# Optimization experiments

Measured on AMD Instinct MI355X. Metric: run time of the kernel, lower is better.

The kernel has to match this reference:

```python
import jax, jax.numpy as jnp
import numpy as np
from jax import lax

G = 8      # deform groups (weight groups == offset groups)
K = 3      # kernel size
K2 = K * K


def conv3x3(x, w, b):
    # NCHW, 3x3, stride 1, padding 1 (SAME)
    y = lax.conv_general_dilated(x, w, (1, 1), 'SAME',
                                 dimension_numbers=('NCHW', 'OIHW', 'NCHW'))
    return y + b[None, :, None, None]


def deform_conv2d(ref, offsets, w, b):
    # ref: [B,C,H,W], offsets: [B,2*G*K2,H,W] (torchvision layout: per group,
    # per kernel position, (dy, dx) pairs), w: [C_out, C_in/G, K, K], b: [C_out]
    B, C, H, W = ref.shape
    Cg = C // G
    off = offsets.reshape(B, G, K2, 2, H, W)
    dy = off[:, :, :, 0]  # [B,G,K2,H,W]
    dx = off[:, :, :, 1]
    ky = (jnp.arange(K2) // K - K // 2).astype(ref.dtype)  # kernel y offsets (pad=1)
    kx = (jnp.arange(K2) % K - K // 2).astype(ref.dtype)
    base_y = jnp.arange(H, dtype=ref.dtype)[:, None] + ky[:, None, None]  # [K2,H,1]
    base_x = jnp.arange(W, dtype=ref.dtype)[None, :] + kx[:, None, None]  # [K2,1,W]
    py = dy + base_y  # [B,G,K2,H,W]
    px = dx + base_x

    y0 = jnp.floor(py).astype(jnp.int32)
    x0 = jnp.floor(px).astype(jnp.int32)
    ly = py - y0.astype(ref.dtype)
    lx = px - x0.astype(ref.dtype)

    ref_flat = ref.reshape(B, G, Cg, H * W)

    def gather(yi, xi):
        valid = (yi >= 0) & (yi < H) & (xi >= 0) & (xi < W)
        idx = jnp.clip(yi, 0, H - 1) * W + jnp.clip(xi, 0, W - 1)  # [B,G,K2,H,W]
        vals = jnp.take_along_axis(ref_flat, idx.reshape(B, G, 1, K2 * H * W), axis=3)
        vals = vals.reshape(B, G, Cg, K2, H, W)
        return vals * valid[:, :, None].astype(ref.dtype)

    w00 = ((1 - ly) * (1 - lx))[:, :, None]
    w01 = ((1 - ly) * lx)[:, :, None]
    w10 = (ly * (1 - lx))[:, :, None]
    w11 = (ly * lx)[:, :, None]
    sampled = (w00 * gather(y0, x0) + w01 * gather(y0, x0 + 1)
               + w10 * gather(y0 + 1, x0) + w11 * gather(y0 + 1, x0 + 1))
    # grouped accumulation: weight [C_out, Cg, K, K] -> [G, OCg, Cg, K2]
    wg = w.reshape(G, C // G, Cg, K2)
    out = jnp.einsum('bgikhw,goik->bgohw', sampled, wg)
    return out.reshape(B, C, H, W) + b[None, :, None, None]


def setup_inputs() -> dict:
    key = jax.random.key(0)
    ks = jax.random.split(key, 10)
    B, C, H, W = 2, 64, 256, 256
    s64 = 1.0 / np.sqrt(C * 9)
    s128 = 1.0 / np.sqrt(128 * 9)
    return {
        'offset': jax.random.normal(ks[0], (B, C, H, W), jnp.float32),
        'ref': jax.random.normal(ks[1], (B, C, H, W), jnp.float32),
        'w_off': jax.random.normal(ks[2], (2 * K2 * G, C, K, K), jnp.float32) * s64,
        'b_off': jnp.zeros((2 * K2 * G,), jnp.float32),
        'w_def': jax.random.normal(ks[3], (C, C // G, K, K), jnp.float32) * (1.0 / np.sqrt((C // G) * 9)),
        'b_def': jnp.zeros((C,), jnp.float32),
        'w_r1': jax.random.normal(ks[4], (C, 2 * C, K, K), jnp.float32) * s128,
        'b_r1': jnp.zeros((C,), jnp.float32),
        'w_r2': jax.random.normal(ks[5], (C, C, K, K), jnp.float32) * s64,
        'b_r2': jnp.zeros((C,), jnp.float32),
    }


def reference(offset, ref, w_off, b_off, w_def, b_def, w_r1, b_r1, w_r2, b_r2):
    deform_offsets = conv3x3(offset, w_off, b_off)              # [B,144,H,W]
    aligned_ref = deform_conv2d(ref, deform_offsets, w_def, b_def)
    x = jnp.concatenate([ref, aligned_ref], axis=1)             # [B,128,H,W]
    x = jax.nn.relu(conv3x3(x, w_r1, b_r1))
    x = jax.nn.relu(conv3x3(x, w_r2, b_r2))
    return x + aligned_ref
```

## Files before the change

kernel.cpp:

```cpp
#include <hip/hip_runtime.h>

typedef __attribute__((ext_vector_type(8)))  short  short8;
typedef __attribute__((ext_vector_type(4)))  float  float4v;
typedef __attribute__((ext_vector_type(16))) float  float16v;
typedef __attribute__((ext_vector_type(2)))  float  f32x2;

constexpr int HH = 256, WW = 256;
constexpr int PD = 258;
constexpr int PR = 260;
constexpr size_t HWsz = (size_t)HH * WW;

__device__ inline unsigned short f2bf(float f) {
    unsigned int u = __builtin_bit_cast(unsigned int, f);
    u += 0x7FFFu + ((u >> 16) & 1u);
    return (unsigned short)(u >> 16);
}
__device__ inline float bfhalf(unsigned int w, int hi) {
    return __builtin_bit_cast(float, hi ? (w & 0xFFFF0000u) : (w << 16));
}
__device__ inline f32x2 unpk2(unsigned int w) {
    f32x2 r;
    r.x = __builtin_bit_cast(float, w << 16);
    r.y = __builtin_bit_cast(float, w & 0xFFFF0000u);
    return r;
}
__device__ inline f32x2 splat2(float s) { f32x2 r; r.x = s; r.y = s; return r; }

template<int CDST, bool WRITE_G>
__global__ __launch_bounds__(256) void nchw_to_nhwc(
    const float* __restrict__ src, unsigned short* __restrict__ dst,
    unsigned short* __restrict__ dst_g)
{
    const int px = threadIdx.x, h = blockIdx.x, bi = blockIdx.y;
    const float* s = src + (size_t)bi * 64 * HWsz + (size_t)h * WW + px;
    unsigned short* d = dst + (((size_t)bi * PD + (h + 1)) * PD + (px + 1)) * CDST;
#pragma unroll
    for (int cg = 0; cg < 8; ++cg) {
        float v[8];
#pragma unroll
        for (int j = 0; j < 8; ++j) v[j] = s[(size_t)(cg * 8 + j) * HWsz];
        uint4 pk;
        pk.x = f2bf(v[0]) | ((unsigned)f2bf(v[1]) << 16);
        pk.y = f2bf(v[2]) | ((unsigned)f2bf(v[3]) << 16);
        pk.z = f2bf(v[4]) | ((unsigned)f2bf(v[5]) << 16);
        pk.w = f2bf(v[6]) | ((unsigned)f2bf(v[7]) << 16);
        *(uint4*)&d[cg * 8] = pk;
        if (WRITE_G) {
            unsigned short* dg = dst_g +
                ((size_t)(bi * 8 + cg) * PR * PR + (size_t)(h + 1) * PR + (px + 1)) * 8;
            *(uint4*)dg = pk;
        }
    }
}

__global__ __launch_bounds__(256) void zero_border(
    unsigned short* __restrict__ p_off, unsigned short* __restrict__ p_cat,
    unsigned short* __restrict__ p_x1, unsigned short* __restrict__ refg)
{
    const int bi = blockIdx.y, which = blockIdx.z;
    if (which == 3) {
        const int total = 8 * 1548;
        for (int i = blockIdx.x * 256 + threadIdx.x; i < total; i += gridDim.x * 256) {
            int g = i / 1548, t = i - g * 1548;
            int r, c;
            if (t < 780)  { int rr = t / 260; c = t - rr * 260; r = rr == 0 ? 0 : 256 + rr; }
            else          { int u = t - 780; int cc = u >> 8; r = 1 + (u & 255); c = cc == 0 ? 0 : 256 + cc; }
            uint4 z = {0, 0, 0, 0};
            *(uint4*)&refg[((size_t)(bi * 8 + g) * PR * PR + (size_t)r * PR + c) * 8] = z;
        }
        return;
    }
    unsigned short* buf = which == 0 ? p_off : (which == 1 ? p_cat : p_x1);
    const int CIN = (which == 1) ? 128 : 64;
    const int NG = CIN / 8;
    unsigned short* p = buf + (size_t)bi * PD * PD * CIN;
    const int total = 1028 * 16;
    for (int i = blockIdx.x * 256 + threadIdx.x; i < total; i += gridDim.x * 256) {
        int g = i & 15;
        if (g >= NG) continue;
        int pxi = i >> 4;
        int r, c;
        if (pxi < 258)       { r = 0;   c = pxi; }
        else if (pxi < 516)  { r = 257; c = pxi - 258; }
        else if (pxi < 772)  { r = pxi - 516 + 1; c = 0; }
        else                 { r = pxi - 772 + 1; c = 257; }
        uint4 z = {0, 0, 0, 0};
        *(uint4*)&p[((size_t)r * PD + c) * CIN + g * 8] = z;
    }
}

__device__ inline void pack_one(const float* __restrict__ w, short* __restrict__ wpk,
                                int Cout, int Cin, int e)
{
    int j = e & 7;
    int lane = (e >> 3) & 63;
    int ksp = 9 * (Cin / 16);
    int kstep = (e >> 9) % ksp;
    int cot = (e >> 9) / ksp;
    int tap = kstep / (Cin / 16);
    int ci = (kstep % (Cin / 16)) * 16 + (lane >> 5) * 8 + j;
    int co = cot * 32 + (lane & 31);
    float v = (co < Cout) ? w[((size_t)co * Cin + ci) * 9 + tap] : 0.f;
    wpk[e] = (short)f2bf(v);
}

__global__ __launch_bounds__(256) void pack_all(
    const float* __restrict__ w1, short* __restrict__ d1,
    const float* __restrict__ w2, short* __restrict__ d2,
    const float* __restrict__ w3, short* __restrict__ d3)
{
    int e = blockIdx.x * 256 + threadIdx.x;
    if (e < 110592)               pack_one(w1, d1, 144, 64, e);
    else if (e < 110592 + 73728)  pack_one(w2, d2, 64, 128, e - 110592);
    else if (e < 221184)          pack_one(w3, d3, 64, 64,  e - 184320);
}

template<int CIN, int COF, int COTB, int MODE, int MINW>
__global__ __launch_bounds__(256, MINW) void conv_mfma_nb(
    const unsigned short* __restrict__ src,
    const short* __restrict__ wpk,
    const float* __restrict__ bias,
    unsigned short* __restrict__ dst_bf,
    float* __restrict__ dst_f,
    const unsigned short* __restrict__ resid_bf)
{
    constexpr int CHUNKS = CIN / 32;
    constexpr int KST = 9 * (CIN / 16);
    constexpr int WSEG = 3 * 4 * 66 * 8;

    __shared__ unsigned short lds[4 * WSEG];

    const int tid  = threadIdx.x;
    const int lane = tid & 63;
    const int wv   = tid >> 6;
    const int half = lane >> 5;
    const int n32  = lane & 31;
    const int h  = blockIdx.x;
    const int bi = blockIdx.y / COTB;
    const int cb = blockIdx.y % COTB;
    const int cbase = cb * COF * 32;

    unsigned short* my = lds + wv * WSEG;
    const unsigned short* srcB = src + (size_t)bi * PD * PD * CIN;
    const short8* wbase = (const short8*)wpk;

    float16v acc[COF][2];
#pragma unroll
    for (int f = 0; f < COF; ++f) {
        float16v bv;
#pragma unroll
        for (int reg = 0; reg < 16; ++reg) {
            int co = cbase + f * 32 + (reg >> 2) * 8 + 4 * half + (reg & 3);
            float b = 0.f;
            if (MODE != 0 || co < 144) b = bias[co];
            bv[reg] = b;
        }
        acc[f][0] = bv;
        acc[f][1] = bv;
    }

    for (int ch = 0; ch < CHUNKS; ++ch) {
        const unsigned short* gband = srcB + ((size_t)h * PD + wv * 64) * CIN + ch * 32;
#pragma unroll
        for (int i0 = 0; i0 < 264; i0 += 64) {
            int i = i0 + lane;
            if (i0 + 64 > 264 && i >= 264) continue;
            int px = i >> 2, o = i & 3;
#pragma unroll
            for (int r = 0; r < 3; ++r) {
                uint4 v = *(const uint4*)(gband + ((size_t)r * PD + px) * CIN + o * 8);
                *(uint4*)&my[(((size_t)r * 4 + o) * 66 + px) * 8] = v;
            }
        }

        short8 abuf[3][COF];
#pragma unroll
        for (int p = 0; p < 2; ++p) {
            const int kp = (p >> 1) * (CIN / 16) + ch * 2 + (p & 1);
#pragma unroll
            for (int f = 0; f < COF; ++f)
                abuf[p][f] = wbase[((size_t)(cb * COF + f) * KST + kp) * 64 + lane];
        }
#pragma unroll
        for (int t = 0; t < 18; ++t) {
            const int tap = t >> 1, s = t & 1;
            const int row = tap / 3, dxo = tap % 3;
            if (t + 2 < 18) {
                const int t2 = t + 2;
                const int k2 = (t2 >> 1) * (CIN / 16) + ch * 2 + (t2 & 1);
#pragma unroll
                for (int f = 0; f < COF; ++f)
                    abuf[t2 % 3][f] = wbase[((size_t)(cb * COF + f) * KST + k2) * 64 + lane];
            }
#pragma unroll
            for (int nt = 0; nt < 2; ++nt) {
                short8 b = *(const short8*)
                    &my[(((size_t)row * 4 + s * 2 + half) * 66 + nt * 32 + dxo + n32) * 8];
#pragma unroll
                for (int f = 0; f < COF; ++f)
                    acc[f][nt] = __builtin_amdgcn_mfma_f32_32x32x16_bf16(abuf[t % 3][f], b, acc[f][nt], 0, 0, 0);
            }
        }
    }

#pragma unroll
    for (int f = 0; f < COF; ++f) {
#pragma unroll
        for (int nt = 0; nt < 2; ++nt) {
            const int px = wv * 64 + nt * 32 + n32;
            float16v a = acc[f][nt];
#pragma unroll
            for (int q = 0; q < 4; ++q) {
                const int co4 = cbase + f * 32 + q * 8 + 4 * half;
                float v0 = a[q * 4 + 0], v1 = a[q * 4 + 1];
                float v2 = a[q * 4 + 2], v3 = a[q * 4 + 3];
                if (MODE == 0) {
                    if (co4 < 144) {
                        unsigned g = ((unsigned)co4 * 3641u) >> 16;
                        unsigned c = (unsigned)co4 - g * 18u;
                        unsigned lo = f2bf(v0) | ((unsigned)f2bf(v1) << 16);
                        unsigned hi = f2bf(v2) | ((unsigned)f2bf(v3) << 16);
                        unsigned short* rec = dst_bf +
                            (((size_t)(bi * 8 + g) * HWsz) + (size_t)h * WW + px) * 18;
                        if (c <= 14) {
                            *(unsigned*)&rec[c]     = lo;
                            *(unsigned*)&rec[c + 2] = hi;
                        } else {
                            *(unsigned*)&rec[16] = lo;
                            unsigned short* rec2 = dst_bf +
                                (((size_t)(bi * 8 + g + 1) * HWsz) + (size_t)h * WW + px) * 18;
                            *(unsigned*)&rec2[0] = hi;
                        }
                    }
                } else if (MODE == 1) {
                    unsigned short* d = dst_bf + (size_t)bi * PD * PD * 64;
                    uint2 pk;
                    pk.x = f2bf(fmaxf(v0, 0.f)) | ((unsigned)f2bf(fmaxf(v1, 0.f)) << 16);
                    pk.y = f2bf(fmaxf(v2, 0.f)) | ((unsigned)f2bf(fmaxf(v3, 0.f)) << 16);
                    *(uint2*)&d[(((size_t)h + 1) * PD + (px + 1)) * 64 + co4] = pk;
                } else {
                    const unsigned short* rp = resid_bf + (size_t)bi * PD * PD * 128;
                    uint2 rv = *(const uint2*)&rp[(((size_t)h + 1) * PD + (px + 1)) * 128 + 64 + co4];
                    float r0 = bfhalf(rv.x, 0), r1 = bfhalf(rv.x, 1);
                    float r2 = bfhalf(rv.y, 0), r3 = bfhalf(rv.y, 1);
                    float* d = dst_f + (size_t)bi * 64 * HWsz + (size_t)h * WW + px;
                    d[(size_t)(co4 + 0) * HWsz] = fmaxf(v0, 0.f) + r0;
                    d[(size_t)(co4 + 1) * HWsz] = fmaxf(v1, 0.f) + r1;
                    d[(size_t)(co4 + 2) * HWsz] = fmaxf(v2, 0.f) + r2;
                    d[(size_t)(co4 + 3) * HWsz] = fmaxf(v3, 0.f) + r3;
                }
            }
        }
    }
}

#define DTAP(DWK, HF, ACC)                                                    \
    {                                                                         \
        float dy = bfhalf(DWK, 0);                                            \
        float dx = bfhalf(DWK, 1);                                            \
        float py  = dy + ((HF) + (float)(k / 3 - 1));                         \
        float pxs = dx + (pxf + (float)(k % 3 - 1));                          \
        py  = fminf(fmaxf(py,  -1.f), 256.f);                                 \
        pxs = fminf(fmaxf(pxs, -1.f), 256.f);                                 \
        float fy = floorf(py), fx = floorf(pxs);                              \
        float ly = py - fy, lx = pxs - fx;                                    \
        int i00 = ((int)fy + 1) * PR + ((int)fx + 1);                         \
        float omly = 1.f - ly, omlx = 1.f - lx;                               \
        f32x2 W00 = splat2(omly * omlx), W01 = splat2(omly * lx);             \
        f32x2 W10 = splat2(ly * omlx),  W11 = splat2(ly * lx);                \
        const uint4 q00 = *(const uint4*)(rb + (size_t)i00 * 8);              \
        const uint4 q01 = *(const uint4*)(rb + (size_t)(i00 + 1) * 8);        \
        const uint4 q10 = *(const uint4*)(rb + (size_t)(i00 + PR) * 8);       \
        const uint4 q11 = *(const uint4*)(rb + (size_t)(i00 + PR + 1) * 8);   \
        union U { uint4 v; unsigned int a[4]; };                              \
        U u00{q00}, u01{q01}, u10{q10}, u11{q11};                             \
        _Pragma("unroll")                                                     \
        for (int cw = 0; cw < 4; ++cw) {                                      \
            f32x2 sv = unpk2(u00.a[cw]) * W00;                                \
            sv = __builtin_elementwise_fma(unpk2(u01.a[cw]), W01, sv);        \
            sv = __builtin_elementwise_fma(unpk2(u10.a[cw]), W10, sv);        \
            sv = __builtin_elementwise_fma(unpk2(u11.a[cw]), W11, sv);        \
            f32x2 bx = splat2(sv.x);                                          \
            f32x2 by = splat2(sv.y);                                          \
            const f32x2* wpa = (const f32x2*)&wsm2[((k * 8) + cw * 2) * 8];   \
            const f32x2* wpb = (const f32x2*)&wsm2[((k * 8) + cw * 2 + 1) * 8];\
            _Pragma("unroll")                                                 \
            for (int o = 0; o < 4; ++o) {                                     \
                ACC[o] = __builtin_elementwise_fma(wpa[o], bx, ACC[o]);       \
                ACC[o] = __builtin_elementwise_fma(wpb[o], by, ACC[o]);       \
            }                                                                 \
        }                                                                     \
    }

__global__ __launch_bounds__(256) void deform_k11(
    const unsigned short* __restrict__ refg,
    const unsigned short* __restrict__ doff,
    const float* __restrict__ wdef, const float* __restrict__ bdef,
    unsigned short* __restrict__ pcat_out)
{
    __shared__ float wsm2[576];
    const int L = blockIdx.x;
    const int xcd = L & 7;
    const int j = L >> 3;
    const int g = j & 7;
    const int r = (j >> 3) & 15;
    const int bi = j >> 7;
    const int h0 = xcd * 32 + r * 2;
    const int px = threadIdx.x;

    for (int i = threadIdx.x; i < 576; i += 256) {
        int o = i & 7, c = (i >> 3) & 7, k = i >> 6;
        wsm2[i] = wdef[(size_t)g * 576 + o * 72 + c * 9 + k];
    }
    __syncthreads();

    const unsigned int* dpA = (const unsigned int*)(
        doff + (((size_t)(bi * 8 + g) * HWsz) + (size_t)h0 * WW + px) * 18);
    const unsigned int* dpB = (const unsigned int*)(
        doff + (((size_t)(bi * 8 + g) * HWsz) + (size_t)(h0 + 1) * WW + px) * 18);
    unsigned int dwA[9], dwB[9];
#pragma unroll
    for (int k = 0; k < 9; ++k) dwA[k] = dpA[k];
#pragma unroll
    for (int k = 0; k < 9; ++k) dwB[k] = dpB[k];

    f32x2 accA[4], accB[4];
#pragma unroll
    for (int o = 0; o < 4; ++o) {
        accA[o].x = bdef[g * 8 + 2 * o];
        accA[o].y = bdef[g * 8 + 2 * o + 1];
        accB[o] = accA[o];
    }

    const unsigned short* rb = refg + (size_t)(bi * 8 + g) * PR * PR * 8;
    const float hfA = (float)h0, hfB = (float)(h0 + 1), pxf = (float)px;

#pragma unroll
    for (int k = 0; k < 9; ++k) {
        DTAP(dwA[k], hfA, accA)
        DTAP(dwB[k], hfB, accB)
    }

    unsigned short* poA = pcat_out + (((size_t)bi * PD + (h0 + 1)) * PD + (px + 1)) * 128 + 64 + g * 8;
    unsigned short* poB = pcat_out + (((size_t)bi * PD + (h0 + 2)) * PD + (px + 1)) * 128 + 64 + g * 8;
    uint4 pkA, pkB;
    pkA.x = f2bf(accA[0].x) | ((unsigned)f2bf(accA[0].y) << 16);
    pkA.y = f2bf(accA[1].x) | ((unsigned)f2bf(accA[1].y) << 16);
    pkA.z = f2bf(accA[2].x) | ((unsigned)f2bf(accA[2].y) << 16);
    pkA.w = f2bf(accA[3].x) | ((unsigned)f2bf(accA[3].y) << 16);
    pkB.x = f2bf(accB[0].x) | ((unsigned)f2bf(accB[0].y) << 16);
    pkB.y = f2bf(accB[1].x) | ((unsigned)f2bf(accB[1].y) << 16);
    pkB.z = f2bf(accB[2].x) | ((unsigned)f2bf(accB[2].y) << 16);
    pkB.w = f2bf(accB[3].x) | ((unsigned)f2bf(accB[3].y) << 16);
    *(uint4*)poA = pkA;
    *(uint4*)poB = pkB;
}

extern "C" void kernel_launch(void* const* d_in, const int* in_sizes, int n_in,
                              void* d_out, int out_size, void* d_ws, size_t ws_size,
                              hipStream_t stream)
{
    const float* offset = (const float*)d_in[0];
    const float* ref    = (const float*)d_in[1];
    const float* w_off  = (const float*)d_in[2];
    const float* b_off  = (const float*)d_in[3];
    const float* w_def  = (const float*)d_in[4];
    const float* b_def  = (const float*)d_in[5];
    const float* w_r1   = (const float*)d_in[6];
    const float* b_r1   = (const float*)d_in[7];
    const float* w_r2   = (const float*)d_in[8];
    const float* b_r2   = (const float*)d_in[9];
    float* out = (float*)d_out;

    unsigned short* p_off = (unsigned short*)d_ws;
    unsigned short* p_cat = p_off + (size_t)8520192;
    unsigned short* p_x1  = p_cat + (size_t)17040384;
    unsigned short* doff  = p_x1 + (size_t)8520192;
    unsigned short* refg  = doff + (size_t)18874368;
    short* wpk1  = (short*)(refg + (size_t)8652800);
    short* wpkr1 = wpk1 + 110592;
    short* wpkr2 = wpkr1 + 73728;

    zero_border<<<dim3(65, 2, 4), 256, 0, stream>>>(p_off, p_cat, p_x1, refg);

    pack_all<<<dim3((221184 + 255) / 256), 256, 0, stream>>>(
        w_off, wpk1, w_r1, wpkr1, w_r2, wpkr2);

    nchw_to_nhwc<64, false><<<dim3(256, 2), 256, 0, stream>>>(offset, p_off, nullptr);
    nchw_to_nhwc<128, true><<<dim3(256, 2), 256, 0, stream>>>(ref, p_cat, refg);

    conv_mfma_nb<64, 2, 3, 0, 3><<<dim3(256, 6), 256, 0, stream>>>(
        p_off, wpk1, b_off, doff, nullptr, nullptr);

    deform_k11<<<dim3(2048), 256, 0, stream>>>(refg, doff, w_def, b_def, p_cat);

    conv_mfma_nb<128, 2, 1, 1, 3><<<dim3(256, 2), 256, 0, stream>>>(
        p_cat, wpkr1, b_r1, p_x1, nullptr, nullptr);

    conv_mfma_nb<64, 2, 1, 2, 3><<<dim3(256, 2), 256, 0, stream>>>(
        p_x1, wpkr2, b_r2, nullptr, out, p_cat);
}
```

Baseline: 325.2 us.

## Merge prep kernels into one launch and retile refine convs across more blocks

Result: slower. 368.4 us (+13.3%).

```diff
diff --git a/kernel.cpp b/kernel.cpp
--- a/kernel.cpp
+++ b/kernel.cpp
@@ -26,12 +26,27 @@
 }
 __device__ inline f32x2 splat2(float s) { f32x2 r; r.x = s; r.y = s; return r; }
 
+__device__ inline void pack_one(const float* __restrict__ w, short* __restrict__ wpk,
+                                int Cout, int Cin, int e)
+{
+    int j = e & 7;
+    int lane = (e >> 3) & 63;
+    int ksp = 9 * (Cin / 16);
+    int kstep = (e >> 9) % ksp;
+    int cot = (e >> 9) / ksp;
+    int tap = kstep / (Cin / 16);
+    int ci = (kstep % (Cin / 16)) * 16 + (lane >> 5) * 8 + j;
+    int co = cot * 32 + (lane & 31);
+    float v = (co < Cout) ? w[((size_t)co * Cin + ci) * 9 + tap] : 0.f;
+    wpk[e] = (short)f2bf(v);
+}
+
 template<int CDST, bool WRITE_G>
-__global__ __launch_bounds__(256) void nchw_to_nhwc(
-    const float* __restrict__ src, unsigned short* __restrict__ dst,
-    unsigned short* __restrict__ dst_g)
-{
-    const int px = threadIdx.x, h = blockIdx.x, bi = blockIdx.y;
+__device__ inline void nchw_row(const float* __restrict__ src,
+                                unsigned short* __restrict__ dst,
+                                unsigned short* __restrict__ dst_g,
+                                int bi, int h, int px)
+{
     const float* s = src + (size_t)bi * 64 * HWsz + (size_t)h * WW + px;
     unsigned short* d = dst + (((size_t)bi * PD + (h + 1)) * PD + (px + 1)) * CDST;
 #pragma unroll
@@ -53,66 +68,53 @@
     }
 }
 
-__global__ __launch_bounds__(256) void zero_border(
+__global__ __launch_bounds__(256) void prep(
+    const float* __restrict__ offset, const float* __restrict__ ref,
+    const float* __restrict__ w1, short* __restrict__ d1,
+    const float* __restrict__ w2, short* __restrict__ d2,
+    const float* __restrict__ w3, short* __restrict__ d3,
     unsigned short* __restrict__ p_off, unsigned short* __restrict__ p_cat,
     unsigned short* __restrict__ p_x1, unsigned short* __restrict__ refg)
 {
-    const int bi = blockIdx.y, which = blockIdx.z;
-    if (which == 3) {
+    const int z = blockIdx.z, bi = blockIdx.y;
+    if (z < 3) {
+        unsigned short* buf = z == 0 ? p_off : (z == 1 ? p_cat : p_x1);
+        const int CIN = (z == 1) ? 128 : 64;
+        const int NG = CIN / 8;
+        unsigned short* p = buf + (size_t)bi * PD * PD * CIN;
+        const int total = 1028 * 16;
+        for (int i = blockIdx.x * 256 + threadIdx.x; i < total; i += gridDim.x * 256) {
+            int g = i & 15;
+            if (g >= NG) continue;
+            int pxi = i >> 4;
+            int r, c;
+            if (pxi < 258)       { r = 0;   c = pxi; }
+            else if (pxi < 516)  { r = 257; c = pxi - 258; }
+            else if (pxi < 772)  { r = pxi - 516 + 1; c = 0; }
+            else                 { r = pxi - 772 + 1; c = 257; }
+            uint4 zv = {0, 0, 0, 0};
+            *(uint4*)&p[((size_t)r * PD + c) * CIN + g * 8] = zv;
+        }
+    } else if (z == 3) {
         const int total = 8 * 1548;
         for (int i = blockIdx.x * 256 + threadIdx.x; i < total; i += gridDim.x * 256) {
             int g = i / 1548, t = i - g * 1548;
             int r, c;
             if (t < 780)  { int rr = t / 260; c = t - rr * 260; r = rr == 0 ? 0 : 256 + rr; }
             else          { int u = t - 780; int cc = u >> 8; r = 1 + (u & 255); c = cc == 0 ? 0 : 256 + cc; }
-            uint4 z = {0, 0, 0, 0};
-            *(uint4*)&refg[((size_t)(bi * 8 + g) * PR * PR + (size_t)r * PR + c) * 8] = z;
-        }
-        return;
-    }
-    unsigned short* buf = which == 0 ? p_off : (which == 1 ? p_cat : p_x1);
-    const int CIN = (which == 1) ? 128 : 64;
-    const int NG = CIN / 8;
-    unsigned short* p = buf + (size_t)bi * PD * PD * CIN;
-    const int total = 1028 * 16;
-    for (int i = blockIdx.x * 256 + threadIdx.x; i < total; i += gridDim.x * 256) {
-        int g = i & 15;
-        if (g >= NG) continue;
-        int pxi = i >> 4;
-        int r, c;
-        if (pxi < 258)       { r = 0;   c = pxi; }
-        else if (pxi < 516)  { r = 257; c = pxi - 258; }
-        else if (pxi < 772)  { r = pxi - 516 + 1; c = 0; }
-        else                 { r = pxi - 772 + 1; c = 257; }
-        uint4 z = {0, 0, 0, 0};
-        *(uint4*)&p[((size_t)r * PD + c) * CIN + g * 8] = z;
-    }
-}
-
-__device__ inline void pack_one(const float* __restrict__ w, short* __restrict__ wpk,
-                                int Cout, int Cin, int e)
-{
-    int j = e & 7;
-    int lane = (e >> 3) & 63;
-    int ksp = 9 * (Cin / 16);
-    int kstep = (e >> 9) % ksp;
-    int cot = (e >> 9) / ksp;
-    int tap = kstep / (Cin / 16);
-    int ci = (kstep % (Cin / 16)) * 16 + (lane >> 5) * 8 + j;
-    int co = cot * 32 + (lane & 31);
-    float v = (co < Cout) ? w[((size_t)co * Cin + ci) * 9 + tap] : 0.f;
-    wpk[e] = (short)f2bf(v);
-}
-
-__global__ __launch_bounds__(256) void pack_all(
-    const float* __restrict__ w1, short* __restrict__ d1,
-    const float* __restrict__ w2, short* __restrict__ d2,
-    const float* __restrict__ w3, short* __restrict__ d3)
-{
-    int e = blockIdx.x * 256 + threadIdx.x;
-    if (e < 110592)               pack_one(w1, d1, 144, 64, e);
-    else if (e < 110592 + 73728)  pack_one(w2, d2, 64, 128, e - 110592);
-    else if (e < 221184)          pack_one(w3, d3, 64, 64,  e - 184320);
+            uint4 zv = {0, 0, 0, 0};
+            *(uint4*)&refg[((size_t)(bi * 8 + g) * PR * PR + (size_t)r * PR + c) * 8] = zv;
+        }
+    } else if (z == 4) {
+        nchw_row<64, false>(offset, p_off, nullptr, bi, blockIdx.x, threadIdx.x);
+    } else if (z == 5) {
+        nchw_row<128, true>(ref, p_cat, refg, bi, blockIdx.x, threadIdx.x);
+    } else {
+        int e = ((z - 6) * 2 + bi) * 65536 + blockIdx.x * 256 + threadIdx.x;
+        if (e < 110592)               pack_one(w1, d1, 144, 64, e);
+        else if (e < 110592 + 73728)  pack_one(w2, d2, 64, 128, e - 110592);
+        else if (e < 221184)          pack_one(w3, d3, 64, 64,  e - 184320);
+    }
 }
 
 template<int CIN, int COF, int COTB, int MODE, int MINW>
@@ -381,22 +383,18 @@
     short* wpkr1 = wpk1 + 110592;
     short* wpkr2 = wpkr1 + 73728;
 
-    zero_border<<<dim3(65, 2, 4), 256, 0, stream>>>(p_off, p_cat, p_x1, refg);
-
-    pack_all<<<dim3((221184 + 255) / 256), 256, 0, stream>>>(
-        w_off, wpk1, w_r1, wpkr1, w_r2, wpkr2);
-
-    nchw_to_nhwc<64, false><<<dim3(256, 2), 256, 0, stream>>>(offset, p_off, nullptr);
-    nchw_to_nhwc<128, true><<<dim3(256, 2), 256, 0, stream>>>(ref, p_cat, refg);
+    prep<<<dim3(256, 2, 8), 256, 0, stream>>>(
+        offset, ref, w_off, wpk1, w_r1, wpkr1, w_r2, wpkr2,
+        p_off, p_cat, p_x1, refg);
 
     conv_mfma_nb<64, 2, 3, 0, 3><<<dim3(256, 6), 256, 0, stream>>>(
         p_off, wpk1, b_off, doff, nullptr, nullptr);
 
     deform_k11<<<dim3(2048), 256, 0, stream>>>(refg, doff, w_def, b_def, p_cat);
 
-    conv_mfma_nb<128, 2, 1, 1, 3><<<dim3(256, 2), 256, 0, stream>>>(
+    conv_mfma_nb<128, 1, 2, 1, 3><<<dim3(256, 4), 256, 0, stream>>>(
         p_cat, wpkr1, b_r1, p_x1, nullptr, nullptr);
 
-    conv_mfma_nb<64, 2, 1, 2, 3><<<dim3(256, 2), 256, 0, stream>>>(
+    conv_mfma_nb<64, 1, 2, 2, 3><<<dim3(256, 4), 256, 0, stream>>>(
         p_x1, wpkr2, b_r2, nullptr, out, p_cat);
 }
```
